# Kernel optimization log

Measured on AMD Instinct MI355X. Metric: run time of the kernel, lower is better.

Reference implementation:

```python
import jax, jax.numpy as jnp
import numpy as np

NHEADS = 16
LN_EPS = 1e-5


def setup_inputs() -> dict:
    key = jax.random.key(0)
    ks = jax.random.split(key, 12)
    B, L, D = 8, 1024, 1024
    bound = 1.0 / np.sqrt(D)
    inp = {
        'query': jax.random.normal(ks[0], (B, L, D), jnp.float32),
        'key':   jax.random.normal(ks[1], (B, L, D), jnp.float32),
        'value': jax.random.normal(ks[2], (B, L, D), jnp.float32),
        'q_mask': jnp.ones((B, L), jnp.float32),
        'k_mask': jnp.ones((B, L), jnp.float32),
        'Wq': jax.random.uniform(ks[3], (D, D), jnp.float32, -bound, bound),
        'bq': jax.random.uniform(ks[4], (D,), jnp.float32, -bound, bound),
        'Wk': jax.random.uniform(ks[5], (D, D), jnp.float32, -bound, bound),
        'bk': jax.random.uniform(ks[6], (D,), jnp.float32, -bound, bound),
        'Wv': jax.random.uniform(ks[7], (D, D), jnp.float32, -bound, bound),
        'bv': jax.random.uniform(ks[8], (D,), jnp.float32, -bound, bound),
        'Wo': jax.random.uniform(ks[9], (D, D), jnp.float32, -bound, bound),
        'bo': jax.random.uniform(ks[10], (D,), jnp.float32, -bound, bound),
        'gamma': jnp.ones((D,), jnp.float32),
        'beta': jnp.zeros((D,), jnp.float32),
    }
    return inp


def reference(query, key, value, q_mask, k_mask, Wq, bq, Wk, bk, Wv, bv, Wo, bo, gamma, beta):
    B, L, D = query.shape
    H = NHEADS
    d = D // H
    residual = query
    # linear projections (torch Linear: x @ W.T + b)
    q = query @ Wq.T + bq
    k = key @ Wk.T + bk
    v = value @ Wv.T + bv
    # NOTE: module does a raw contiguous view [B, L, H*d] -> [B*H, L, d]
    # (NOT a transpose-based head split). Replicate exactly.
    q = q.reshape(B * H, L, d)
    k = k.reshape(B * H, L, d)
    v = v.reshape(B * H, L, d)
    # masks tiled head-major: repeat(nheads, 1) -> [H*B, L]
    qm = jnp.tile(q_mask, (H, 1))
    km = jnp.tile(k_mask, (H, 1))
    mask = qm[:, :, None] * km[:, None, :]  # [B*H, L, L] outer product
    scores = jnp.einsum('bqd,bkd->bqk', q, k) / np.sqrt(d).astype(np.float32)
    A = jnp.exp(jnp.where(mask == 0, -jnp.inf, scores))  # unstable exp, as in source
    A_sum = jnp.clip(jnp.sum(A, axis=-1, keepdims=True), 2e-15, None)
    attn = A / A_sum
    context = (attn @ v).reshape(B, L, H * d)
    out = context @ Wo.T + bo
    # dropout is identity in eval mode
    x = residual + out
    mean = jnp.mean(x, axis=-1, keepdims=True)
    var = jnp.mean(jnp.square(x - mean), axis=-1, keepdims=True)
    return (x - mean) / jnp.sqrt(var + LN_EPS) * gamma + beta
```

## Files before the change

### kernel.cpp

```cpp
#include <hip/hip_runtime.h>
#include <hip/hip_bf16.h>


typedef __bf16 bf16x8 __attribute__((ext_vector_type(8)));
typedef float  f32x4  __attribute__((ext_vector_type(4)));

#define KK 1024
#define NN 1024

union BfPack4 { __bf16 h[4]; uint2 u; };
union BfPack8 { __bf16 h[8]; uint4 u; };

__device__ __forceinline__ void lds_copy16(void* lds, const void* gsrc) {
  __builtin_amdgcn_global_load_lds(
      (__attribute__((address_space(1))) void*)(uintptr_t)gsrc,
      (__attribute__((address_space(3))) void*)(unsigned int)(uintptr_t)lds,
      16, 0, 0);
}

struct Cvt4 { const float* src[4]; __bf16* dst; };

__global__ __launch_bounds__(256) void cvt_w(Cvt4 a) {
  const int z = blockIdx.y;
  const float* s = a.src[z];
  __bf16* d = a.dst + (size_t)z * (KK * NN);
  const int i = (blockIdx.x * 256 + threadIdx.x) * 4;
  float4 f = *(const float4*)&s[i];
  BfPack4 p;
  p.h[0] = (__bf16)f.x; p.h[1] = (__bf16)f.y;
  p.h[2] = (__bf16)f.z; p.h[3] = (__bf16)f.w;
  *(uint2*)&d[i] = p.u;
}

struct GQKV {
  const float*  A[3];
  const __bf16* W;
  const float*  bias[3];
  __bf16*       C[3];
};

__global__ __launch_bounds__(256) void gemm_qkv(GQKV args)
{
  __shared__ alignas(16) __bf16 As[128 * 40];
  __shared__ alignas(16) __bf16 Bs[2][4096];
  const int z = blockIdx.z;
  const float*  A    = args.A[z];
  const __bf16* W    = args.W + (size_t)z * KK * NN;
  const float*  bias = args.bias[z];
  __bf16* C = args.C[z];
  const int tid = threadIdx.x, l = tid & 63, w = tid >> 6;
  const int m0 = blockIdx.x * 128, n0 = blockIdx.y * 128;
  const int lr = l & 15, lq = l >> 4;
  const int wm = (w & 1) * 64, wn = (w >> 1) * 64;

  const __bf16* gw0 = &W[(size_t)(n0 + (tid >> 2)) * KK + (tid & 3) * 8];
  const __bf16* gw1 = &W[(size_t)(n0 + 64 + (tid >> 2)) * KK + (tid & 3) * 8];

  float4 pa[4];
  #pragma unroll
  for (int s = 0; s < 4; ++s) {
    int c = tid + 256 * s; int row = c >> 3, ko = (c & 7) * 4;
    pa[s] = *(const float4*)&A[(size_t)(m0 + row) * KK + ko];
  }
  lds_copy16((char*)Bs + w * 1024,        gw0);
  lds_copy16((char*)Bs + 4096 + w * 1024, gw1);

  f32x4 acc[4][4] = {};
  int ib = 0;
  for (int kk = 0; kk < KK; kk += 32) {
    __syncthreads();
    #pragma unroll
    for (int s = 0; s < 4; ++s) {
      int c = tid + 256 * s; int row = c >> 3, ko = (c & 7) * 4;
      BfPack4 p;
      p.h[0] = (__bf16)pa[s].x; p.h[1] = (__bf16)pa[s].y;
      p.h[2] = (__bf16)pa[s].z; p.h[3] = (__bf16)pa[s].w;
      *(uint2*)&As[row * 40 + ko] = p.u;
    }
    __syncthreads();
    if (kk + 32 < KK) {
      lds_copy16((char*)Bs + (ib ^ 1) * 8192 + w * 1024,        gw0 + kk + 32);
      lds_copy16((char*)Bs + (ib ^ 1) * 8192 + 4096 + w * 1024, gw1 + kk + 32);
      #pragma unroll
      for (int s = 0; s < 4; ++s) {
        int c = tid + 256 * s; int row = c >> 3, ko = (c & 7) * 4;
        pa[s] = *(const float4*)&A[(size_t)(m0 + row) * KK + kk + 32 + ko];
      }
    }
    const __bf16* Bb = (const __bf16*)((char*)Bs + ib * 8192);
    bf16x8 af[4], bf[4];
    #pragma unroll
    for (int t = 0; t < 4; ++t) {
      af[t] = *(const bf16x8*)&As[(wm + t * 16 + lr) * 40 + lq * 8];
      bf[t] = *(const bf16x8*)&Bb[(wn + t * 16 + lr) * 32 + lq * 8];
    }
    #pragma unroll
    for (int mt = 0; mt < 4; ++mt)
      #pragma unroll
      for (int nt = 0; nt < 4; ++nt)
        acc[mt][nt] = __builtin_amdgcn_mfma_f32_16x16x32_bf16(af[mt], bf[nt], acc[mt][nt], 0, 0, 0);
    ib ^= 1;
  }

  #pragma unroll
  for (int mt = 0; mt < 4; ++mt)
    #pragma unroll
    for (int nt = 0; nt < 4; ++nt)
      #pragma unroll
      for (int i = 0; i < 4; ++i) {
        int gm = m0 + wm + mt * 16 + lq * 4 + i;
        int gn = n0 + wn + nt * 16 + lr;
        C[(size_t)gm * NN + gn] = (__bf16)(acc[mt][nt][i] + bias[gn]);
      }
}

struct GO { const __bf16* A; const __bf16* W; const float* bias; float* C; };

__global__ __launch_bounds__(256) void gemm_out(GO args)
{
  __shared__ alignas(16) __bf16 As[2][4096];
  __shared__ alignas(16) __bf16 Bs[2][4096];
  const int tid = threadIdx.x, l = tid & 63, w = tid >> 6;
  const int m0 = blockIdx.x * 128, n0 = blockIdx.y * 128;
  const int lr = l & 15, lq = l >> 4;
  const int wm = (w & 1) * 64, wn = (w >> 1) * 64;

  const __bf16* ga0 = &args.A[(size_t)(m0 + (tid >> 2)) * KK + (tid & 3) * 8];
  const __bf16* ga1 = &args.A[(size_t)(m0 + 64 + (tid >> 2)) * KK + (tid & 3) * 8];
  const __bf16* gw0 = &args.W[(size_t)(n0 + (tid >> 2)) * KK + (tid & 3) * 8];
  const __bf16* gw1 = &args.W[(size_t)(n0 + 64 + (tid >> 2)) * KK + (tid & 3) * 8];

  lds_copy16((char*)As + w * 1024,        ga0);
  lds_copy16((char*)As + 4096 + w * 1024, ga1);
  lds_copy16((char*)Bs + w * 1024,        gw0);
  lds_copy16((char*)Bs + 4096 + w * 1024, gw1);

  f32x4 acc[4][4] = {};
  int ib = 0;
  for (int kk = 0; kk < KK; kk += 32) {
    __syncthreads();
    if (kk + 32 < KK) {
      lds_copy16((char*)As + (ib ^ 1) * 8192 + w * 1024,        ga0 + kk + 32);
      lds_copy16((char*)As + (ib ^ 1) * 8192 + 4096 + w * 1024, ga1 + kk + 32);
      lds_copy16((char*)Bs + (ib ^ 1) * 8192 + w * 1024,        gw0 + kk + 32);
      lds_copy16((char*)Bs + (ib ^ 1) * 8192 + 4096 + w * 1024, gw1 + kk + 32);
    }
    const __bf16* Ab = (const __bf16*)((char*)As + ib * 8192);
    const __bf16* Bb = (const __bf16*)((char*)Bs + ib * 8192);
    bf16x8 af[4], bf[4];
    #pragma unroll
    for (int t = 0; t < 4; ++t) {
      af[t] = *(const bf16x8*)&Ab[(wm + t * 16 + lr) * 32 + lq * 8];
      bf[t] = *(const bf16x8*)&Bb[(wn + t * 16 + lr) * 32 + lq * 8];
    }
    #pragma unroll
    for (int mt = 0; mt < 4; ++mt)
      #pragma unroll
      for (int nt = 0; nt < 4; ++nt)
        acc[mt][nt] = __builtin_amdgcn_mfma_f32_16x16x32_bf16(af[mt], bf[nt], acc[mt][nt], 0, 0, 0);
    ib ^= 1;
  }

  #pragma unroll
  for (int mt = 0; mt < 4; ++mt)
    #pragma unroll
    for (int nt = 0; nt < 4; ++nt)
      #pragma unroll
      for (int i = 0; i < 4; ++i) {
        int gm = m0 + wm + mt * 16 + lq * 4 + i;
        int gn = n0 + wn + nt * 16 + lr;
        args.C[(size_t)gm * NN + gn] = acc[mt][nt][i] + args.bias[gn];
      }
}

__global__ __launch_bounds__(256) void attn_kernel(
    const __bf16* __restrict__ qb, const __bf16* __restrict__ kb,
    const __bf16* __restrict__ vb, const float* __restrict__ qm,
    const float* __restrict__ km, __bf16* __restrict__ ctxb)
{
  const int g  = blockIdx.y;
  const int qt = blockIdx.x;
  const int tid = threadIdx.x, l = tid & 63, w = tid >> 6;
  const int lr = l & 15, lq = l >> 4;

  __shared__ alignas(16) __bf16 Ps[128 * 72];
  __shared__ alignas(16) __bf16 Ks[2 * 128 * 32];
  __shared__ alignas(16) __bf16 Vt[64 * 136];
  __shared__ alignas(16) __bf16 kms[1024];

  const size_t gbase = (size_t)g * (1024 * 64);
  const __bf16* qg = qb + gbase;
  const __bf16* kg = kb + gbase;
  const __bf16* vg = vb + gbase;
  const float* qmrow = qm + (size_t)(g & 7) * 1024;
  const float* kmrow = km + (size_t)(g & 7) * 1024;

  #pragma unroll
  for (int s = 0; s < 4; ++s) {
    int c = tid + 256 * s;
    int p = c >> 9, r = (c >> 2) & 127, q0 = c & 3;
    lds_copy16((char*)Ps + w * 1024 + s * 4096,
               &qg[(size_t)(qt * 128 + r) * 64 + p * 32 + q0 * 8]);
  }
  {
    float4 kf = *(const float4*)&kmrow[tid * 4];
    BfPack4 p;
    p.h[0] = (__bf16)(kf.x == 0.f ? 0.f : 1.f);
    p.h[1] = (__bf16)(kf.y == 0.f ? 0.f : 1.f);
    p.h[2] = (__bf16)(kf.z == 0.f ? 0.f : 1.f);
    p.h[3] = (__bf16)(kf.w == 0.f ? 0.f : 1.f);
    *(uint2*)&kms[tid * 4] = p.u;
  }
  float qmv[2][4];
  #pragma unroll
  for (int rt = 0; rt < 2; ++rt)
    #pragma unroll
    for (int i = 0; i < 4; ++i)
      qmv[rt][i] = qmrow[qt * 128 + 32 * w + rt * 16 + lq * 4 + i];

  __syncthreads();

  bf16x8 qa[2][2];
  #pragma unroll
  for (int rt = 0; rt < 2; ++rt)
    #pragma unroll
    for (int p = 0; p < 2; ++p)
      qa[rt][p] = *(const bf16x8*)((char*)Ps + p * 8192 +
                                   (32 * w + rt * 16 + lr) * 64 + lq * 16);

  uint4 pv[4];
  #pragma unroll
  for (int s = 0; s < 4; ++s) {
    int ch = tid + 256 * s; int j = ch & 127, c0 = ch >> 7;
    pv[s] = *(const uint4*)&vg[(size_t)j * 64 + c0 * 8];
  }

  float rs[2][4] = {};
  f32x4 ctx[2][4] = {};

  for (int kt = 0; kt < 8; ++kt) {
    __syncthreads();
    #pragma unroll
    for (int s = 0; s < 4; ++s) {
      int c = tid + 256 * s;
      int p = c >> 9, r = (c >> 2) & 127, q0 = c & 3;
      lds_copy16((char*)Ks + w * 1024 + s * 4096,
                 &kg[(size_t)(kt * 128 + r) * 64 + p * 32 + q0 * 8]);
    }
    #pragma unroll
    for (int s = 0; s < 4; ++s) {
      int ch = tid + 256 * s; int j = ch & 127, c0 = ch >> 7;
      BfPack8 vv; vv.u = pv[s];
      #pragma unroll
      for (int cc = 0; cc < 8; ++cc)
        Vt[(c0 * 8 + cc) * 136 + j] = vv.h[cc];
    }
    __syncthreads();
    if (kt < 7) {
      #pragma unroll
      for (int s = 0; s < 4; ++s) {
        int ch = tid + 256 * s; int j = ch & 127, c0 = ch >> 7;
        pv[s] = *(const uint4*)&vg[(size_t)((kt + 1) * 128 + j) * 64 + c0 * 8];
      }
    }
    const int wkey = 16 * (lq >> 1);
    const int rkey = 16 * ((lr >> 3) & 1);
    #pragma unroll
    for (int h = 0; h < 2; ++h) {
      f32x4 sacc[2][4];
      #pragma unroll
      for (int c4 = 0; c4 < 4; ++c4) {
        int ct = h * 4 + c4;
        bf16x8 kb0 = *(const bf16x8*)((char*)Ks + (ct * 16 + lr) * 64 + lq * 16);
        bf16x8 kb1 = *(const bf16x8*)((char*)Ks + 8192 + (ct * 16 + lr) * 64 + lq * 16);
        #pragma unroll
        for (int rt = 0; rt < 2; ++rt) {
          f32x4 zz = {};
          zz = __builtin_amdgcn_mfma_f32_16x16x32_bf16(qa[rt][0], kb0, zz, 0, 0, 0);
          sacc[rt][c4] = __builtin_amdgcn_mfma_f32_16x16x32_bf16(qa[rt][1], kb1, zz, 0, 0, 0);
        }
      }
      #pragma unroll
      for (int c4 = 0; c4 < 4; ++c4) {
        int ct = h * 4 + c4;
        float kmv = (float)kms[kt * 128 + ct * 16 + lr];
        #pragma unroll
        for (int rt = 0; rt < 2; ++rt)
          #pragma unroll
          for (int i = 0; i < 4; ++i) {
            float e = (qmv[rt][i] * kmv == 0.f) ? 0.f
                                                : __expf(sacc[rt][c4][i] * 0.125f);
            rs[rt][i] += e;
            int row = 32 * w + rt * 16 + lq * 4 + i;
            Ps[row * 72 + ((c4 * 16 + lr) ^ wkey)] = (__bf16)e;
          }
      }
      #pragma unroll
      for (int ks = 0; ks < 2; ++ks) {
        bf16x8 pa[2];
        #pragma unroll
        for (int rt = 0; rt < 2; ++rt)
          pa[rt] = *(const bf16x8*)&Ps[(32 * w + rt * 16 + lr) * 72 +
                                       ((ks * 32 + lq * 8) ^ rkey)];
        #pragma unroll
        for (int c2 = 0; c2 < 4; ++c2) {
          bf16x8 vf = *(const bf16x8*)&Vt[(c2 * 16 + lr) * 136 +
                                          h * 64 + ks * 32 + lq * 8];
          #pragma unroll
          for (int rt = 0; rt < 2; ++rt)
            ctx[rt][c2] = __builtin_amdgcn_mfma_f32_16x16x32_bf16(pa[rt], vf, ctx[rt][c2], 0, 0, 0);
        }
      }
    }
  }

  #pragma unroll
  for (int rt = 0; rt < 2; ++rt)
    #pragma unroll
    for (int i = 0; i < 4; ++i) {
      float v = rs[rt][i];
      v += __shfl_xor(v, 1);
      v += __shfl_xor(v, 2);
      v += __shfl_xor(v, 4);
      v += __shfl_xor(v, 8);
      rs[rt][i] = 1.0f / fmaxf(v, 2e-15f);
    }

  #pragma unroll
  for (int rt = 0; rt < 2; ++rt)
    #pragma unroll
    for (int c2 = 0; c2 < 4; ++c2)
      #pragma unroll
      for (int i = 0; i < 4; ++i) {
        int row = qt * 128 + 32 * w + rt * 16 + lq * 4 + i;
        ctxb[gbase + (size_t)row * 64 + c2 * 16 + lr] =
            (__bf16)(ctx[rt][c2][i] * rs[rt][i]);
      }
}

__global__ __launch_bounds__(256) void ln_kernel(
    const float* __restrict__ O, const float* __restrict__ resid,
    const float* __restrict__ gam, const float* __restrict__ bet,
    float* __restrict__ out)
{
  const int row = blockIdx.x;
  const int tid = threadIdx.x;
  const float* orow = O + (size_t)row * 1024;
  const float* rrow = resid + (size_t)row * 1024;
  float x[4];
  float sum = 0.f, sq = 0.f;
  #pragma unroll
  for (int j = 0; j < 4; ++j) {
    int c = tid + j * 256;
    x[j] = orow[c] + rrow[c];
    sum += x[j];
    sq  += x[j] * x[j];
  }
  #pragma unroll
  for (int off = 32; off > 0; off >>= 1) {
    sum += __shfl_down(sum, off, 64);
    sq  += __shfl_down(sq, off, 64);
  }
  __shared__ float s1[4], s2[4];
  __shared__ float mean_s, inv_s;
  if ((tid & 63) == 0) { s1[tid >> 6] = sum; s2[tid >> 6] = sq; }
  __syncthreads();
  if (tid == 0) {
    float S = s1[0] + s1[1] + s1[2] + s1[3];
    float Q = s2[0] + s2[1] + s2[2] + s2[3];
    float mean = S * (1.0f / 1024.0f);
    float var  = fmaxf(Q * (1.0f / 1024.0f) - mean * mean, 0.0f);
    mean_s = mean;
    inv_s  = rsqrtf(var + 1e-5f);
  }
  __syncthreads();
  float mean = mean_s, inv = inv_s;
  #pragma unroll
  for (int j = 0; j < 4; ++j) {
    int c = tid + j * 256;
    out[(size_t)row * 1024 + c] = (x[j] - mean) * inv * gam[c] + bet[c];
  }
}

extern "C" void kernel_launch(void* const* d_in, const int* in_sizes, int n_in,
                              void* d_out, int out_size, void* d_ws, size_t ws_size,
                              hipStream_t stream)
{
  const float* query = (const float*)d_in[0];
  const float* keyi  = (const float*)d_in[1];
  const float* value = (const float*)d_in[2];
  const float* qmask = (const float*)d_in[3];
  const float* kmask = (const float*)d_in[4];
  const float* Wq = (const float*)d_in[5];
  const float* bq = (const float*)d_in[6];
  const float* Wk = (const float*)d_in[7];
  const float* bk = (const float*)d_in[8];
  const float* Wv = (const float*)d_in[9];
  const float* bv = (const float*)d_in[10];
  const float* Wo = (const float*)d_in[11];
  const float* bo = (const float*)d_in[12];
  const float* gam = (const float*)d_in[13];
  const float* bet = (const float*)d_in[14];

  char* ws = (char*)d_ws;
  __bf16* qbuf = (__bf16*)(ws);
  __bf16* kbuf = (__bf16*)(ws + ((size_t)16 << 20));
  __bf16* vbuf = (__bf16*)(ws + ((size_t)32 << 20));
  __bf16* wb   = (__bf16*)(ws + ((size_t)48 << 20));
  float*  obuf = (float*)(ws + ((size_t)16 << 20));

  Cvt4 cv;
  cv.src[0] = Wq; cv.src[1] = Wk; cv.src[2] = Wv; cv.src[3] = Wo;
  cv.dst = wb;

  GQKV qkv;
  qkv.A[0] = query; qkv.A[1] = keyi; qkv.A[2] = value;
  qkv.W = wb;
  qkv.bias[0] = bq; qkv.bias[1] = bk; qkv.bias[2] = bv;
  qkv.C[0] = qbuf;  qkv.C[1] = kbuf; qkv.C[2] = vbuf;

  GO op;
  op.A = qbuf;
  op.W = wb + (size_t)3 * KK * NN;
  op.bias = bo;
  op.C = obuf;

  dim3 tb(256);
  hipLaunchKernelGGL(cvt_w, dim3(1024, 4), tb, 0, stream, cv);
  hipLaunchKernelGGL(gemm_qkv, dim3(64, 8, 3), tb, 0, stream, qkv);
  hipLaunchKernelGGL(attn_kernel, dim3(8, 128), tb, 0, stream, qbuf, kbuf, vbuf, qmask, kmask, qbuf);
  hipLaunchKernelGGL(gemm_out, dim3(64, 8), tb, 0, stream, op);
  hipLaunchKernelGGL(ln_kernel, dim3(8192), tb, 0, stream, obuf, query, gam, bet, (float*)d_out);
}
```

Before: 401.9 us.

## Replace GEMMs with 256x256-tile, 8-wave, ping-pong scheduled bf16 GEMM kernel

Adds a new GEMM kernel with 256x256 tiles, 512 threads, 128KB LDS double buffering, XOR-swizzled LDS layout, block-index remapping, and barrier/setprio-interleaved staging and MFMA phases. The output projection always uses it. The QKV projection uses it only when the workspace is large enough, in which case activations are first converted to bf16 by a separate pass. This aims to raise arithmetic intensity and MFMA utilisation, at the cost of an extra conversion kernel and much higher LDS use per block (fewer blocks per CU).

```diff
diff --git a/kernel.cpp b/kernel.cpp
--- a/kernel.cpp
+++ b/kernel.cpp
@@ -30,6 +30,183 @@
   p.h[0] = (__bf16)f.x; p.h[1] = (__bf16)f.y;
   p.h[2] = (__bf16)f.z; p.h[3] = (__bf16)f.w;
   *(uint2*)&d[i] = p.u;
+}
+
+struct Cvt3 { const float* src[3]; __bf16* dst; };
+
+__global__ __launch_bounds__(256) void cvt_a(Cvt3 a) {
+  const int z = blockIdx.y;
+  const float* s = a.src[z];
+  __bf16* d = a.dst + (size_t)z * ((size_t)8 << 20);
+  const size_t i = ((size_t)blockIdx.x * 256 + threadIdx.x) * 8;
+  float4 f0 = *(const float4*)&s[i];
+  float4 f1 = *(const float4*)&s[i + 4];
+  BfPack8 p;
+  p.h[0] = (__bf16)f0.x; p.h[1] = (__bf16)f0.y;
+  p.h[2] = (__bf16)f0.z; p.h[3] = (__bf16)f0.w;
+  p.h[4] = (__bf16)f1.x; p.h[5] = (__bf16)f1.y;
+  p.h[6] = (__bf16)f1.z; p.h[7] = (__bf16)f1.w;
+  *(uint4*)&d[i] = p.u;
+}
+
+struct G8 {
+  const __bf16* A[3];
+  const __bf16* W[3];
+  const float*  bias[3];
+  void*         C[3];
+};
+
+#define BAR()   __builtin_amdgcn_s_barrier()
+#define PRIO(x) __builtin_amdgcn_s_setprio(x)
+#define WAIT_LGKM0() do { asm volatile("s_waitcnt lgkmcnt(0)" ::: "memory"); \
+                          __builtin_amdgcn_sched_barrier(0); } while (0)
+#define WAIT_VM4()  asm volatile("s_waitcnt vmcnt(4)" ::: "memory")
+#define WAIT_VM0()  asm volatile("s_waitcnt vmcnt(0)" ::: "memory")
+
+#define STAGE_A(buf, half, kt) do {                                          \
+  lds_copy16(smem + (buf)*32768 + (half)*16384 + ldsW,                       \
+             pA0[half] + (size_t)(kt)*64);                                   \
+  lds_copy16(smem + (buf)*32768 + (half)*16384 + ldsW + 1024,                \
+             pA1[half] + (size_t)(kt)*64); } while (0)
+
+#define STAGE_B(buf, half, kt) do {                                          \
+  lds_copy16(smem + 65536 + (buf)*32768 + (half)*16384 + ldsW,               \
+             pB0[half] + (size_t)(kt)*64);                                   \
+  lds_copy16(smem + 65536 + (buf)*32768 + (half)*16384 + ldsW + 1024,        \
+             pB1[half] + (size_t)(kt)*64); } while (0)
+
+#define LDA(buf, mh) do {                                                    \
+  const char* _p = aSelf + (buf)*32768 + (mh)*8192;                          \
+  _Pragma("unroll") for (int i_ = 0; i_ < 4; ++i_) {                         \
+    af[i_][0] = *(const bf16x8*)(_p + i_*2048 + c0_);                        \
+    af[i_][1] = *(const bf16x8*)(_p + i_*2048 + c1_); } } while (0)
+
+#define LDB(buf, nh) do {                                                    \
+  const char* _p = bSelf + (buf)*32768 + (nh)*4096;                          \
+  _Pragma("unroll") for (int j_ = 0; j_ < 2; ++j_) {                         \
+    bf[(nh)*2 + j_][0] = *(const bf16x8*)(_p + j_*2048 + c0_);               \
+    bf[(nh)*2 + j_][1] = *(const bf16x8*)(_p + j_*2048 + c1_); } } while (0)
+
+#define MM(mh, nh) do {                                                      \
+  _Pragma("unroll") for (int i_ = 0; i_ < 4; ++i_)                           \
+  _Pragma("unroll") for (int j_ = 0; j_ < 2; ++j_) {                         \
+    acc[(mh)*4+i_][(nh)*2+j_] = __builtin_amdgcn_mfma_f32_16x16x32_bf16(     \
+        af[i_][0], bf[(nh)*2+j_][0], acc[(mh)*4+i_][(nh)*2+j_], 0, 0, 0);    \
+    acc[(mh)*4+i_][(nh)*2+j_] = __builtin_amdgcn_mfma_f32_16x16x32_bf16(     \
+        af[i_][1], bf[(nh)*2+j_][1], acc[(mh)*4+i_][(nh)*2+j_], 0, 0, 0);    \
+  } } while (0)
+
+template <bool OUT_BF16>
+__global__ __launch_bounds__(512, 2) void gemm8p(G8 args)
+{
+  __shared__ __align__(16) char smem[131072];
+  const int z = blockIdx.z;
+  const __bf16* __restrict__ A    = args.A[z];
+  const __bf16* __restrict__ W    = args.W[z];
+  const float*  __restrict__ bias = args.bias[z];
+
+  const int tid = threadIdx.x;
+  const int l = tid & 63, w = tid >> 6;
+  const int lr = l & 15, lq = l >> 4;
+  const int wr = w >> 2, wc = w & 3;
+
+  int lin = blockIdx.y * 32 + blockIdx.x;
+  lin = (lin & 7) * 16 + (lin >> 3);
+  const int m0 = (lin & 31) * 256;
+  const int n0 = (lin >> 5) * 256;
+
+  const int s0 = w * 128 + l, s1 = s0 + 64;
+  const int r0 = s0 >> 3, kq0 = (s0 & 7) ^ (r0 & 7);
+  const int r1 = s1 >> 3, kq1 = (s1 & 7) ^ (r1 & 7);
+  const __bf16* pA0[2]; const __bf16* pA1[2];
+  const __bf16* pB0[2]; const __bf16* pB1[2];
+  #pragma unroll
+  for (int h = 0; h < 2; ++h) {
+    pA0[h] = A + (size_t)(m0 + h * 128 + r0) * KK + kq0 * 8;
+    pA1[h] = A + (size_t)(m0 + h * 128 + r1) * KK + kq1 * 8;
+    pB0[h] = W + (size_t)(n0 + h * 128 + r0) * KK + kq0 * 8;
+    pB1[h] = W + (size_t)(n0 + h * 128 + r1) * KK + kq1 * 8;
+  }
+  const int ldsW = w * 2048;
+
+  const int aRow = lr * 128;
+  const int c0_ = ((lq)     ^ (lr & 7)) * 16;
+  const int c1_ = ((4 + lq) ^ (lr & 7)) * 16;
+  const char* aSelf = smem + wr * 16384 + aRow;
+  const char* bSelf = smem + 65536 + (wc >> 1) * 16384 + (wc & 1) * 8192 + aRow;
+
+  bf16x8 af[4][2], bf[4][2];
+  f32x4 acc[8][4] = {};
+
+  STAGE_A(0, 0, 0); STAGE_A(0, 1, 0);
+  STAGE_B(0, 0, 0); STAGE_B(0, 1, 0);
+  STAGE_B(1, 0, 1); STAGE_B(1, 1, 1);
+  WAIT_VM4();
+  BAR();
+
+  for (int it = 0; it < 8; ++it) {
+    const int t2 = it * 2;
+    LDA(0, 0); LDB(0, 0);
+    STAGE_A(1, 0, t2 + 1);
+    BAR(); WAIT_LGKM0();
+    PRIO(1); MM(0, 0); PRIO(0);
+    BAR();
+    LDB(0, 1);
+    STAGE_A(1, 1, t2 + 1);
+    BAR(); WAIT_LGKM0();
+    PRIO(1); MM(0, 1); PRIO(0);
+    BAR();
+    LDA(0, 1);
+    if (it < 7) STAGE_B(0, 0, t2 + 2);
+    BAR(); WAIT_LGKM0();
+    PRIO(1); MM(1, 0); PRIO(0);
+    BAR();
+    if (it < 7) { STAGE_B(0, 1, t2 + 2); WAIT_VM4(); }
+    else        { WAIT_VM0(); }
+    BAR();
+    PRIO(1); MM(1, 1); PRIO(0);
+    BAR();
+    LDA(1, 0); LDB(1, 0);
+    if (it < 7) STAGE_A(0, 0, t2 + 2);
+    BAR(); WAIT_LGKM0();
+    PRIO(1); MM(0, 0); PRIO(0);
+    BAR();
+    LDB(1, 1);
+    if (it < 7) STAGE_A(0, 1, t2 + 2);
+    BAR(); WAIT_LGKM0();
+    PRIO(1); MM(0, 1); PRIO(0);
+    BAR();
+    LDA(1, 1);
+    if (it < 7) STAGE_B(1, 0, t2 + 3);
+    BAR(); WAIT_LGKM0();
+    PRIO(1); MM(1, 0); PRIO(0);
+    BAR();
+    if (it < 7) { STAGE_B(1, 1, t2 + 3); WAIT_VM4(); }
+    BAR();
+    PRIO(1); MM(1, 1); PRIO(0);
+    BAR();
+  }
+
+  float bv[4];
+  #pragma unroll
+  for (int n = 0; n < 4; ++n) bv[n] = bias[n0 + wc * 64 + n * 16 + lr];
+
+  #pragma unroll
+  for (int f = 0; f < 8; ++f) {
+    const int gm = m0 + wr * 128 + f * 16 + lq * 4;
+    #pragma unroll
+    for (int n = 0; n < 4; ++n) {
+      const int gn = n0 + wc * 64 + n * 16 + lr;
+      #pragma unroll
+      for (int i = 0; i < 4; ++i) {
+        const float v = acc[f][n][i] + bv[n];
+        if constexpr (OUT_BF16)
+          ((__bf16*)args.C[z])[(size_t)(gm + i) * NN + gn] = (__bf16)v;
+        else
+          ((float*)args.C[z])[(size_t)(gm + i) * NN + gn] = v;
+      }
+    }
+  }
 }
 
 struct GQKV {
@@ -88,17 +265,17 @@
       }
     }
     const __bf16* Bb = (const __bf16*)((char*)Bs + ib * 8192);
-    bf16x8 af[4], bf[4];
+    bf16x8 af2[4], bf2[4];
     #pragma unroll
     for (int t = 0; t < 4; ++t) {
-      af[t] = *(const bf16x8*)&As[(wm + t * 16 + lr) * 40 + lq * 8];
-      bf[t] = *(const bf16x8*)&Bb[(wn + t * 16 + lr) * 32 + lq * 8];
+      af2[t] = *(const bf16x8*)&As[(wm + t * 16 + lr) * 40 + lq * 8];
+      bf2[t] = *(const bf16x8*)&Bb[(wn + t * 16 + lr) * 32 + lq * 8];
     }
     #pragma unroll
     for (int mt = 0; mt < 4; ++mt)
       #pragma unroll
       for (int nt = 0; nt < 4; ++nt)
-        acc[mt][nt] = __builtin_amdgcn_mfma_f32_16x16x32_bf16(af[mt], bf[nt], acc[mt][nt], 0, 0, 0);
+        acc[mt][nt] = __builtin_amdgcn_mfma_f32_16x16x32_bf16(af2[mt], bf2[nt], acc[mt][nt], 0, 0, 0);
     ib ^= 1;
   }
 
@@ -111,65 +288,6 @@
         int gm = m0 + wm + mt * 16 + lq * 4 + i;
         int gn = n0 + wn + nt * 16 + lr;
         C[(size_t)gm * NN + gn] = (__bf16)(acc[mt][nt][i] + bias[gn]);
-      }
-}
-
-struct GO { const __bf16* A; const __bf16* W; const float* bias; float* C; };
-
-__global__ __launch_bounds__(256) void gemm_out(GO args)
-{
-  __shared__ alignas(16) __bf16 As[2][4096];
-  __shared__ alignas(16) __bf16 Bs[2][4096];
-  const int tid = threadIdx.x, l = tid & 63, w = tid >> 6;
-  const int m0 = blockIdx.x * 128, n0 = blockIdx.y * 128;
-  const int lr = l & 15, lq = l >> 4;
-  const int wm = (w & 1) * 64, wn = (w >> 1) * 64;
-
-  const __bf16* ga0 = &args.A[(size_t)(m0 + (tid >> 2)) * KK + (tid & 3) * 8];
-  const __bf16* ga1 = &args.A[(size_t)(m0 + 64 + (tid >> 2)) * KK + (tid & 3) * 8];
-  const __bf16* gw0 = &args.W[(size_t)(n0 + (tid >> 2)) * KK + (tid & 3) * 8];
-  const __bf16* gw1 = &args.W[(size_t)(n0 + 64 + (tid >> 2)) * KK + (tid & 3) * 8];
-
-  lds_copy16((char*)As + w * 1024,        ga0);
-  lds_copy16((char*)As + 4096 + w * 1024, ga1);
-  lds_copy16((char*)Bs + w * 1024,        gw0);
-  lds_copy16((char*)Bs + 4096 + w * 1024, gw1);
-
-  f32x4 acc[4][4] = {};
-  int ib = 0;
-  for (int kk = 0; kk < KK; kk += 32) {
-    __syncthreads();
-    if (kk + 32 < KK) {
-      lds_copy16((char*)As + (ib ^ 1) * 8192 + w * 1024,        ga0 + kk + 32);
-      lds_copy16((char*)As + (ib ^ 1) * 8192 + 4096 + w * 1024, ga1 + kk + 32);
-      lds_copy16((char*)Bs + (ib ^ 1) * 8192 + w * 1024,        gw0 + kk + 32);
-      lds_copy16((char*)Bs + (ib ^ 1) * 8192 + 4096 + w * 1024, gw1 + kk + 32);
-    }
-    const __bf16* Ab = (const __bf16*)((char*)As + ib * 8192);
-    const __bf16* Bb = (const __bf16*)((char*)Bs + ib * 8192);
-    bf16x8 af[4], bf[4];
-    #pragma unroll
-    for (int t = 0; t < 4; ++t) {
-      af[t] = *(const bf16x8*)&Ab[(wm + t * 16 + lr) * 32 + lq * 8];
-      bf[t] = *(const bf16x8*)&Bb[(wn + t * 16 + lr) * 32 + lq * 8];
-    }
-    #pragma unroll
-    for (int mt = 0; mt < 4; ++mt)
-      #pragma unroll
-      for (int nt = 0; nt < 4; ++nt)
-        acc[mt][nt] = __builtin_amdgcn_mfma_f32_16x16x32_bf16(af[mt], bf[nt], acc[mt][nt], 0, 0, 0);
-    ib ^= 1;
-  }
-
-  #pragma unroll
-  for (int mt = 0; mt < 4; ++mt)
-    #pragma unroll
-    for (int nt = 0; nt < 4; ++nt)
-      #pragma unroll
-      for (int i = 0; i < 4; ++i) {
-        int gm = m0 + wm + mt * 16 + lq * 4 + i;
-        int gn = n0 + wn + nt * 16 + lr;
-        args.C[(size_t)gm * NN + gn] = acc[mt][nt][i] + args.bias[gn];
       }
 }
 
@@ -231,8 +349,8 @@
   uint4 pv[4];
   #pragma unroll
   for (int s = 0; s < 4; ++s) {
-    int ch = tid + 256 * s; int j = ch & 127, c0 = ch >> 7;
-    pv[s] = *(const uint4*)&vg[(size_t)j * 64 + c0 * 8];
+    int ch = tid + 256 * s; int j = ch & 127, cc0 = ch >> 7;
+    pv[s] = *(const uint4*)&vg[(size_t)j * 64 + cc0 * 8];
   }
 
   float rs[2][4] = {};
@@ -249,18 +367,18 @@
     }
     #pragma unroll
     for (int s = 0; s < 4; ++s) {
-      int ch = tid + 256 * s; int j = ch & 127, c0 = ch >> 7;
+      int ch = tid + 256 * s; int j = ch & 127, cc0 = ch >> 7;
       BfPack8 vv; vv.u = pv[s];
       #pragma unroll
       for (int cc = 0; cc < 8; ++cc)
-        Vt[(c0 * 8 + cc) * 136 + j] = vv.h[cc];
+        Vt[(cc0 * 8 + cc) * 136 + j] = vv.h[cc];
     }
     __syncthreads();
     if (kt < 7) {
       #pragma unroll
       for (int s = 0; s < 4; ++s) {
-        int ch = tid + 256 * s; int j = ch & 127, c0 = ch >> 7;
-        pv[s] = *(const uint4*)&vg[(size_t)((kt + 1) * 128 + j) * 64 + c0 * 8];
+        int ch = tid + 256 * s; int j = ch & 127, cc0 = ch >> 7;
+        pv[s] = *(const uint4*)&vg[(size_t)((kt + 1) * 128 + j) * 64 + cc0 * 8];
       }
     }
     const int wkey = 16 * (lq >> 1);
@@ -297,18 +415,18 @@
       }
       #pragma unroll
       for (int ks = 0; ks < 2; ++ks) {
-        bf16x8 pa[2];
+        bf16x8 pa2[2];
         #pragma unroll
         for (int rt = 0; rt < 2; ++rt)
-          pa[rt] = *(const bf16x8*)&Ps[(32 * w + rt * 16 + lr) * 72 +
-                                       ((ks * 32 + lq * 8) ^ rkey)];
+          pa2[rt] = *(const bf16x8*)&Ps[(32 * w + rt * 16 + lr) * 72 +
+                                        ((ks * 32 + lq * 8) ^ rkey)];
         #pragma unroll
         for (int c2 = 0; c2 < 4; ++c2) {
           bf16x8 vf = *(const bf16x8*)&Vt[(c2 * 16 + lr) * 136 +
                                           h * 64 + ks * 32 + lq * 8];
           #pragma unroll
           for (int rt = 0; rt < 2; ++rt)
-            ctx[rt][c2] = __builtin_amdgcn_mfma_f32_16x16x32_bf16(pa[rt], vf, ctx[rt][c2], 0, 0, 0);
+            ctx[rt][c2] = __builtin_amdgcn_mfma_f32_16x16x32_bf16(pa2[rt], vf, ctx[rt][c2], 0, 0, 0);
         }
       }
     }
@@ -408,27 +526,52 @@
   __bf16* vbuf = (__bf16*)(ws + ((size_t)32 << 20));
   __bf16* wb   = (__bf16*)(ws + ((size_t)48 << 20));
   float*  obuf = (float*)(ws + ((size_t)16 << 20));
+  __bf16* abuf = (__bf16*)(ws + ((size_t)56 << 20));
+
+  const bool big = ws_size >= ((size_t)104 << 20);
 
   Cvt4 cv;
   cv.src[0] = Wq; cv.src[1] = Wk; cv.src[2] = Wv; cv.src[3] = Wo;
   cv.dst = wb;
 
-  GQKV qkv;
-  qkv.A[0] = query; qkv.A[1] = keyi; qkv.A[2] = value;
-  qkv.W = wb;
-  qkv.bias[0] = bq; qkv.bias[1] = bk; qkv.bias[2] = bv;
-  qkv.C[0] = qbuf;  qkv.C[1] = kbuf; qkv.C[2] = vbuf;
-
-  GO op;
-  op.A = qbuf;
-  op.W = wb + (size_t)3 * KK * NN;
-  op.bias = bo;
-  op.C = obuf;
-
   dim3 tb(256);
   hipLaunchKernelGGL(cvt_w, dim3(1024, 4), tb, 0, stream, cv);
-  hipLaunchKernelGGL(gemm_qkv, dim3(64, 8, 3), tb, 0, stream, qkv);
-  hipLaunchKernelGGL(attn_kernel, dim3(8, 128), tb, 0, stream, qbuf, kbuf, vbuf, qmask, kmask, qbuf);
-  hipLaunchKernelGGL(gemm_out, dim3(64, 8), tb, 0, stream, op);
-  hipLaunchKernelGGL(ln_kernel, dim3(8192), tb, 0, stream, obuf, query, gam, bet, (float*)d_out);
-}
+
+  if (big) {
+    Cvt3 ca;
+    ca.src[0] = query; ca.src[1] = keyi; ca.src[2] = value;
+    ca.dst = abuf;
+    hipLaunchKernelGGL(cvt_a, dim3(4096, 3), tb, 0, stream, ca);
+
+    G8 gq;
+    gq.A[0] = abuf;
+    gq.A[1] = abuf + ((size_t)8 << 20);
+    gq.A[2] = abuf + ((size_t)16 << 20);
+    gq.W[0] = wb; gq.W[1] = wb + (size_t)KK * NN; gq.W[2] = wb + (size_t)2 * KK * NN;
+    gq.bias[0] = bq; gq.bias[1] = bk; gq.bias[2] = bv;
+    gq.C[0] = qbuf; gq.C[1] = kbuf; gq.C[2] = vbuf;
+    hipLaunchKernelGGL((gemm8p<true>), dim3(32, 4, 3), dim3(512), 0, stream, gq);
+  } else {
+    GQKV qkv;
+    qkv.A[0] = query; qkv.A[1] = keyi; qkv.A[2] = value;
+    qkv.W = wb;
+    qkv.bias[0] = bq; qkv.bias[1] = bk; qkv.bias[2] = bv;
+    qkv.C[0] = qbuf;  qkv.C[1] = kbuf; qkv.C[2] = vbuf;
+    hipLaunchKernelGGL(gemm_qkv, dim3(64, 8, 3), tb, 0, stream, qkv);
+  }
+
+  hipLaunchKernelGGL(attn_kernel, dim3(8, 128), tb, 0, stream,
+                     qbuf, kbuf, vbuf, qmask, kmask, qbuf);
+
+  G8 go;
+  go.A[0] = qbuf;
+  go.W[0] = wb + (size_t)3 * KK * NN;
+  go.bias[0] = bo;
+  go.C[0] = obuf;
+  go.A[1] = go.A[2] = go.A[0]; go.W[1] = go.W[2] = go.W[0];
+  go.bias[1] = go.bias[2] = go.bias[0]; go.C[1] = go.C[2] = go.C[0];
+  hipLaunchKernelGGL((gemm8p<false>), dim3(32, 4, 1), dim3(512), 0, stream, go);
+
+  hipLaunchKernelGGL(ln_kernel, dim3(8192), tb, 0, stream,
+                     obuf, query, gam, bet, (float*)d_out);
+}
```

Result: faster. 387.6 us (-3.6%).
